# Optimization experiments

Hardware: AMD Instinct MI355X
Metric: run time of the kernel (lower is better)

Reference implementation:

```python
import jax, jax.numpy as jnp
import numpy as np

DIM = 512
HEADS = 8
HEAD_DIM = DIM // HEADS
SCALE = HEAD_DIM ** -0.5
LN_EPS = 1e-5


def _layernorm(t, g, b):
    mu = jnp.mean(t, axis=-1, keepdims=True)
    var = jnp.mean(jnp.square(t - mu), axis=-1, keepdims=True)
    return (t - mu) * jax.lax.rsqrt(var + LN_EPS) * g + b


def setup_inputs() -> dict:
    key = jax.random.key(0)
    ks = jax.random.split(key, 8)
    B, C, H, W = 2, DIM, 48, 48
    s = 1.0 / np.sqrt(DIM)
    return {
        "x": jax.random.normal(ks[0], (B, C, H, W), jnp.float32),
        "y": jax.random.normal(ks[1], (B, C, H, W), jnp.float32),
        # linear weights stored [in, out]
        "k_w": jax.random.uniform(ks[2], (DIM, DIM), jnp.float32, -s, s),
        "k_b": jax.random.uniform(ks[3], (DIM,), jnp.float32, -s, s),
        "qv_w": jax.random.uniform(ks[4], (DIM, 2 * DIM), jnp.float32, -s, s),
        "qv_b": jax.random.uniform(ks[5], (2 * DIM,), jnp.float32, -s, s),
        "lnx_g": jnp.ones((DIM,), jnp.float32),
        "lnx_b": jnp.zeros((DIM,), jnp.float32),
        "lny_g": jnp.ones((DIM,), jnp.float32),
        "lny_b": jnp.zeros((DIM,), jnp.float32),
    }


def _split_qv(t, qv_w, qv_b):
    B, N, C = t.shape
    qv = (t @ qv_w + qv_b).reshape(B, N, 2, HEADS, HEAD_DIM)
    qv = jnp.transpose(qv, (2, 0, 3, 1, 4))  # [2, B, h, N, d]
    return qv[0], qv[1]


def _heads(t):
    B, N, C = t.shape
    return jnp.transpose(t.reshape(B, N, HEADS, HEAD_DIM), (0, 2, 1, 3))  # [B,h,N,d]


def reference(x, y, k_w, k_b, qv_w, qv_b, lnx_g, lnx_b, lny_g, lny_b):
    B, C = x.shape[0], x.shape[1]
    xf = _layernorm(jnp.transpose(x.reshape(B, C, -1), (0, 2, 1)), lnx_g, lnx_b)  # [B,N,C]
    yf = _layernorm(jnp.transpose(y.reshape(B, C, -1), (0, 2, 1)), lny_g, lny_b)
    N = xf.shape[1]

    y_q, y_v = _split_qv(yf, qv_w, qv_b)
    x_q, x_v = _split_qv(xf, qv_w, qv_b)
    y_k = _heads(yf @ k_w + k_b)
    x_k = _heads(xf @ k_w + k_b)

    # branch 1: softmax(x_q y_k^T) x_v  -> standard [B,N,C]
    a1 = jax.nn.softmax(jnp.einsum('bhnd,bhmd->bhnm', x_q, y_k) * SCALE, axis=-1)
    xo = jnp.einsum('bhnm,bhmd->bhnd', a1, x_v)
    xo = jnp.transpose(xo, (0, 2, 1, 3)).reshape(B, N, C)

    # branch 2: faithful reproduction of torch quirk (x_k kept a leading 1-dim,
    # so the output [1,B,h,N,d].transpose(1,2).reshape(B,N,C) scrambles layout)
    a2 = jax.nn.softmax(jnp.einsum('bhnd,bhmd->bhnm', y_q, x_k) * SCALE, axis=-1)
    yo = jnp.einsum('bhnm,bhmd->bhnd', a2, y_v)  # [B,h,N,d]
    yo = jnp.transpose(yo[None], (0, 2, 1, 3, 4)).reshape(B, N, C)

    return jnp.concatenate([xo, yo], axis=0)  # [2B, N, C]
```

## Files before the change

### kernel.cpp

```cpp
#include <hip/hip_runtime.h>

#define DIM 512
#define NTOK 2304
#define HEADS 8
#define HD 64
#define LN_EPS 1e-5f
#define BNC 2359296
#define QSC 0.18033688011112042f

typedef __attribute__((ext_vector_type(8))) short short8;
typedef __attribute__((ext_vector_type(4))) short sh4;
typedef __attribute__((ext_vector_type(4))) float f32x4;

__device__ __forceinline__ short f2bf(float f) {
    union { float f; unsigned u; } x; x.f = f;
    unsigned r = (x.u + 0x7fffu + ((x.u >> 16) & 1u)) >> 16;
    return (short)(r & 0xffffu);
}
__device__ __forceinline__ unsigned fbits(float f) {
    union { float f; unsigned u; } x; x.f = f; return x.u;
}
__device__ __forceinline__ void gl2lds(const short* g, short* l) {
    __builtin_amdgcn_global_load_lds(
        (const __attribute__((address_space(1))) unsigned int*)g,
        (__attribute__((address_space(3))) unsigned int*)l, 16, 0, 0);
}

__global__ void k_pre(const float* __restrict__ x, const float* __restrict__ y,
                      const float* __restrict__ qv_w, const float* __restrict__ k_w,
                      const float* __restrict__ qv_b, const float* __restrict__ k_b,
                      const float* __restrict__ gx, const float* __restrict__ bx,
                      const float* __restrict__ gy, const float* __restrict__ by,
                      short* __restrict__ T, short* __restrict__ Wt,
                      float* __restrict__ bias) {
    __shared__ __align__(16) float tile[64][65];
    __shared__ float pS[4][64], pQ[4][64];
    __shared__ float muL[64], rsL[64];
    int bkid = blockIdx.x, tid = threadIdx.x;
    if (bkid < 1152) {
        int nt = bkid % 36, ct = (bkid / 36) % 8, sb = bkid / 288;
        int s = sb >> 1, b = sb & 1;
        int n0 = nt * 64, c0 = ct * 64;
        const float* src = (s ? y : x) + (size_t)b * DIM * NTOK;
        int nl = tid & 63, part = tid >> 6;
        {
            const float* p = src + n0 + nl;
            float sum = 0.f, sq = 0.f;
            for (int c = part * 128; c < part * 128 + 128; c++) {
                float v = p[(size_t)c * NTOK];
                sum += v; sq += v * v;
            }
            pS[part][nl] = sum; pQ[part][nl] = sq;
        }
        __syncthreads();
        if (tid < 64) {
            float ts = pS[0][tid] + pS[1][tid] + pS[2][tid] + pS[3][tid];
            float tq = pQ[0][tid] + pQ[1][tid] + pQ[2][tid] + pQ[3][tid];
            float m = ts * (1.0f / DIM);
            float var = tq * (1.0f / DIM) - m * m;
            muL[tid] = m;
            rsL[tid] = rsqrtf(var + LN_EPS);
        }
        for (int slot = tid; slot < 1024; slot += 256) {
            int r = slot >> 4, q = slot & 15;
            const float* p = src + (size_t)(c0 + r) * NTOK + n0 + q * 4;
            float4 v = *(const float4*)p;
            tile[r][q*4+0] = v.x; tile[r][q*4+1] = v.y;
            tile[r][q*4+2] = v.z; tile[r][q*4+3] = v.w;
        }
        __syncthreads();
        const float* g  = s ? gy : gx;
        const float* be = s ? by : bx;
        int nr = tid >> 2, cg = tid & 3;
        float m = muL[nr], r_ = rsL[nr];
        short8 o0, o1;
        for (int i = 0; i < 8; i++) {
            int c = c0 + cg * 16 + i;
            o0[i] = f2bf((tile[cg*16+i][nr] - m) * r_ * g[c] + be[c]);
        }
        for (int i = 0; i < 8; i++) {
            int c = c0 + cg * 16 + 8 + i;
            o1[i] = f2bf((tile[cg*16+8+i][nr] - m) * r_ * g[c] + be[c]);
        }
        short* dst = T + ((size_t)sb * NTOK + n0 + nr) * DIM + c0 + cg * 16;
        *(short8*)dst = o0;
        *(short8*)(dst + 8) = o1;
        return;
    }
    int idx = bkid - 1152;
    int jt = idx % 24, ct = idx / 24;
    int j0 = jt * 64, c0 = ct * 64;
    if (ct == 0 && tid < 64) {
        int j = j0 + tid;
        bias[j] = (j < 1024) ? qv_b[j] : k_b[j - 1024];
    }
    for (int slot = tid; slot < 1024; slot += 256) {
        int r = slot >> 4, q = slot & 15;
        int c = c0 + r;
        float4 v;
        if (j0 < 1024) v = *(const float4*)(qv_w + (size_t)c * 1024 + j0 + q * 4);
        else           v = *(const float4*)(k_w  + (size_t)c * 512  + (j0 - 1024) + q * 4);
        tile[r][q*4+0] = v.x; tile[r][q*4+1] = v.y;
        tile[r][q*4+2] = v.z; tile[r][q*4+3] = v.w;
    }
    __syncthreads();
    int jr = tid >> 2, cg = tid & 3;
    short8 o0, o1;
    for (int i = 0; i < 8; i++) o0[i] = f2bf(tile[cg*16+i][jr]);
    for (int i = 0; i < 8; i++) o1[i] = f2bf(tile[cg*16+8+i][jr]);
    short* dst = Wt + (size_t)(j0 + jr) * DIM + c0 + cg * 16;
    *(short8*)dst = o0;
    *(short8*)(dst + 8) = o1;
}

__global__ void __launch_bounds__(256)
k_gemm(const short* __restrict__ T, const short* __restrict__ Wt,
       const float* __restrict__ bias, short* __restrict__ QVK,
       short* __restrict__ VT) {
    __shared__ __align__(16) short smem[2 * 128 * 64];
    short* As = smem;
    short* Bs = smem + 128 * 64;
    int n0 = blockIdx.x * 128, j0 = blockIdx.y * 128, sb = blockIdx.z;
    int tid = threadIdx.x;
    int w = tid >> 6, l = tid & 63;
    int wr = w >> 1, wc = w & 1;
    int lrow = l & 15, quad = l >> 4;
    int r_in = (l >> 3) & 7, cc = l & 7;
    int ch = cc ^ r_in;
    int sw0 = (quad ^ (lrow & 7)) * 8;
    const short* Ab = T + (size_t)sb * NTOK * DIM;
    f32x4 acc[4][4] = {};
    for (int kk = 0; kk < 8; kk++) {
        if (kk) __syncthreads();
        for (int inst = 0; inst < 4; inst++) {
            int R = w * 32 + inst * 8 + r_in;
            gl2lds(Ab + (size_t)(n0 + R) * 512 + kk * 64 + ch * 8,
                   &As[(w * 32 + inst * 8) * 64]);
            gl2lds(Wt + (size_t)(j0 + R) * 512 + kk * 64 + ch * 8,
                   &Bs[(w * 32 + inst * 8) * 64]);
        }
        __syncthreads();
        for (int c2 = 0; c2 < 2; c2++) {
            int off = c2 ? (sw0 ^ 32) : sw0;
            short8 af[4], bf[4];
            for (int i = 0; i < 4; i++)
                af[i] = *(const short8*)&As[(wr*64 + i*16 + lrow) * 64 + off];
            for (int j = 0; j < 4; j++)
                bf[j] = *(const short8*)&Bs[(wc*64 + j*16 + lrow) * 64 + off];
            for (int i = 0; i < 4; i++)
                for (int j = 0; j < 4; j++)
                    acc[i][j] = __builtin_amdgcn_mfma_f32_16x16x32_bf16(af[i], bf[j], acc[i][j], 0, 0, 0);
        }
    }
    if (j0 >= 512 && j0 < 1024) {
        __syncthreads();
        for (int i = 0; i < 4; i++)
            for (int j = 0; j < 4; j++) {
                int jloc = wc * 64 + j * 16 + lrow;
                float bv = bias[j0 + jloc];
                int nloc = wr * 64 + i * 16 + quad * 4;
                int c8 = nloc >> 3, half = (nloc >> 2) & 1;
                sh4 pk;
                for (int reg = 0; reg < 4; reg++) pk[reg] = f2bf(acc[i][j][reg] + bv);
                *(sh4*)&smem[jloc * 128 + ((c8 ^ (jloc & 15)) * 8) + half * 4] = pk;
            }
        __syncthreads();
        for (int slot = tid; slot < 2048; slot += 256) {
            int row = slot >> 4, seg = slot & 15;
            short8 v = *(const short8*)&smem[row * 128 + ((seg ^ (row & 15)) * 8)];
            *(short8*)(VT + ((size_t)sb * 512 + (j0 - 512) + row) * NTOK + n0 + seg * 8) = v;
        }
    } else {
        for (int i = 0; i < 4; i++)
            for (int j = 0; j < 4; j++) {
                int jj = j0 + wc * 64 + j * 16 + lrow;
                float bv = bias[jj];
                float sc = (jj < 512) ? QSC : 1.0f;
                for (int reg = 0; reg < 4; reg++) {
                    int n = n0 + wr * 64 + i * 16 + quad * 4 + reg;
                    QVK[((size_t)sb * NTOK + n) * 1536 + jj] = f2bf((acc[i][j][reg] + bv) * sc);
                }
            }
    }
}

__global__ void __launch_bounds__(256)
k_attn(const short* __restrict__ QVK, const short* __restrict__ VT,
       float* __restrict__ out, float* __restrict__ O1,
       float* __restrict__ l0, float* __restrict__ l1) {
    __shared__ __align__(16) short Kbuf[2][64 * 64];
    __shared__ __align__(16) short Vbuf[2][64 * 64];
    __shared__ __align__(16) short Qs[64 * 64];
    int id = blockIdx.x;
    int half = id / 1152;
    int rid = id % 1152;
    int xcd = rid & 7, rem = rid >> 3;
    int qt = rem % 36, yhi = rem / 36;
    int yb = yhi * 8 + xcd;
    int br = yb >> 4;
    int b  = (yb >> 3) & 1;
    int h  = yb & 7;
    int tid = threadIdx.x;
    int w = tid >> 6, l = tid & 63;
    int lrow = l & 15, quad = l >> 4;
    int r_in = (l >> 3) & 7, cc = l & 7;
    int ch = cc ^ r_in;
    int sw0 = (quad ^ (lrow & 7)) * 8;
    int n0 = qt * 64;
    int m_base = half * 1152;
    const short* Qg = QVK + ((size_t)(br * 2 + b) * NTOK) * 1536 + h * 64;
    const short* Kg = QVK + ((size_t)((1 - br) * 2 + b) * NTOK) * 1536 + 1024 + h * 64;
    const short* Vg = VT + ((size_t)(br * 2 + b) * 512 + h * 64) * NTOK;

    for (int inst = 0; inst < 2; inst++) {
        int R = w * 16 + inst * 8 + r_in;
        gl2lds(Qg + (size_t)(n0 + R) * 1536 + ch * 8, &Qs[(w * 16 + inst * 8) * 64]);
    }

    const short* KnA = Kg + (size_t)(m_base + w * 16 + r_in) * 1536 + ch * 8;
    const short* KnB = Kg + (size_t)(m_base + w * 16 + 8 + r_in) * 1536 + ch * 8;
    const short* VnA = Vg + (size_t)(w * 16 + r_in) * NTOK + m_base + ch * 8;
    const short* VnB = Vg + (size_t)(w * 16 + 8 + r_in) * NTOK + m_base + ch * 8;
    int lds_off = l * 8;

    short8 ka = *(const short8*)(KnA);
    short8 kb = *(const short8*)(KnB);
    short8 va = *(const short8*)(VnA);
    short8 vb = *(const short8*)(VnB);
    KnA += (size_t)64 * 1536; KnB += (size_t)64 * 1536;
    VnA += 64; VnB += 64;

    __syncthreads();
    short8 bq0 = *(const short8*)&Qs[(w * 16 + lrow) * 64 + sw0];
    short8 bq1 = *(const short8*)&Qs[(w * 16 + lrow) * 64 + (sw0 ^ 32)];
    short* Pw = &Qs[w * 16 * 64];

    *(short8*)&Kbuf[0][(w * 16)     * 64 + lds_off] = ka;
    *(short8*)&Kbuf[0][(w * 16 + 8) * 64 + lds_off] = kb;
    *(short8*)&Vbuf[0][(w * 16)     * 64 + lds_off] = va;
    *(short8*)&Vbuf[0][(w * 16 + 8) * 64 + lds_off] = vb;
    ka = *(const short8*)(KnA);
    kb = *(const short8*)(KnB);
    va = *(const short8*)(VnA);
    vb = *(const short8*)(VnB);
    KnA += (size_t)64 * 1536; KnB += (size_t)64 * 1536;
    VnA += 64; VnB += 64;

    short8 ones;
    for (int i = 0; i < 8; i++) ones[i] = (short)0x3F80;

    f32x4 Oacc[4] = {};
    f32x4 lacc = {};
    int cur = 0;

    for (int mt = 0; mt < 18; mt++) {
        __syncthreads();
        const short* Ks = Kbuf[cur];
        const short* Vs = Vbuf[cur];

        for (int sub = 0; sub < 4; sub++) {
            short8 ak0 = *(const short8*)&Ks[(sub * 16 + lrow) * 64 + sw0];
            short8 ak1 = *(const short8*)&Ks[(sub * 16 + lrow) * 64 + (sw0 ^ 32)];
            f32x4 a = {};
            a = __builtin_amdgcn_mfma_f32_16x16x32_bf16(ak0, bq0, a, 0, 0, 0);
            a = __builtin_amdgcn_mfma_f32_16x16x32_bf16(ak1, bq1, a, 0, 0, 0);
            float p0 = __builtin_amdgcn_exp2f(a[0]), p1 = __builtin_amdgcn_exp2f(a[1]);
            float p2 = __builtin_amdgcn_exp2f(a[2]), p3 = __builtin_amdgcn_exp2f(a[3]);
            uint2 pk;
            pk.x = __builtin_amdgcn_perm(fbits(p1), fbits(p0), 0x07060302u);
            pk.y = __builtin_amdgcn_perm(fbits(p3), fbits(p2), 0x07060302u);
            *(uint2*)&Pw[lrow * 64 + (((2 * sub + (quad >> 1)) ^ (lrow & 7)) * 8) + (quad & 1) * 4] = pk;
        }

        short8 ap0 = *(const short8*)&Pw[lrow * 64 + sw0];
        short8 ap1 = *(const short8*)&Pw[lrow * 64 + (sw0 ^ 32)];
        lacc = __builtin_amdgcn_mfma_f32_16x16x32_bf16(ones, ap0, lacc, 0, 0, 0);
        lacc = __builtin_amdgcn_mfma_f32_16x16x32_bf16(ones, ap1, lacc, 0, 0, 0);
        for (int ddt = 0; ddt < 4; ddt++) {
            short8 av0 = *(const short8*)&Vs[(ddt * 16 + lrow) * 64 + sw0];
            short8 av1 = *(const short8*)&Vs[(ddt * 16 + lrow) * 64 + (sw0 ^ 32)];
            Oacc[ddt] = __builtin_amdgcn_mfma_f32_16x16x32_bf16(av0, ap0, Oacc[ddt], 0, 0, 0);
            Oacc[ddt] = __builtin_amdgcn_mfma_f32_16x16x32_bf16(av1, ap1, Oacc[ddt], 0, 0, 0);
        }

        if (mt + 1 < 18) {
            *(short8*)&Kbuf[cur ^ 1][(w * 16)     * 64 + lds_off] = ka;
            *(short8*)&Kbuf[cur ^ 1][(w * 16 + 8) * 64 + lds_off] = kb;
            *(short8*)&Vbuf[cur ^ 1][(w * 16)     * 64 + lds_off] = va;
            *(short8*)&Vbuf[cur ^ 1][(w * 16 + 8) * 64 + lds_off] = vb;
        }
        if (mt + 2 < 18) {
            ka = *(const short8*)(KnA);
            kb = *(const short8*)(KnB);
            va = *(const short8*)(VnA);
            vb = *(const short8*)(VnB);
        }
        KnA += (size_t)64 * 1536; KnB += (size_t)64 * 1536;
        VnA += 64; VnB += 64;
        cur ^= 1;
    }

    int n = n0 + w * 16 + lrow;
    if (quad == 0) (half ? l1 : l0)[yb * NTOK + n] = lacc[0];
    for (int ddt = 0; ddt < 4; ddt++) {
        float4 o;
        o.x = Oacc[ddt][0];
        o.y = Oacc[ddt][1];
        o.z = Oacc[ddt][2];
        o.w = Oacc[ddt][3];
        if (half == 0) {
            if (br == 0)
                *(float4*)&out[((size_t)b * NTOK + n) * 512 + h * 64 + ddt * 16 + quad * 4] = o;
            else
                *(float4*)&out[(size_t)BNC + ((size_t)(h * 2 + b) * NTOK + n) * 64 + ddt * 16 + quad * 4] = o;
        } else {
            *(float4*)&O1[((size_t)yb * NTOK + n) * 64 + ddt * 16 + quad * 4] = o;
        }
    }
}

__global__ void __launch_bounds__(256)
k_norm(float* __restrict__ out, const float* __restrict__ O1,
       const float* __restrict__ l0, const float* __restrict__ l1) {
    int i = blockIdx.x * 256 + threadIdx.x;
    int o = i * 4;
    int yb, n, d;
    if (o < BNC) {
        int b = o / (NTOK * 512);
        int r = o % (NTOK * 512);
        n = r >> 9;
        int c = r & 511;
        d = c & 63;
        yb = b * 8 + (c >> 6);
    } else {
        int o2 = o - BNC;
        int hb = o2 / (NTOK * 64);
        n = (o2 >> 6) % NTOK;
        d = o2 & 63;
        yb = 16 + (hb & 1) * 8 + (hb >> 1);
    }
    int li = yb * NTOK + n;
    float linv = 1.f / (l0[li] + l1[li]);
    float4 a = *(const float4*)&out[o];
    float4 q = *(const float4*)&O1[(size_t)li * 64 + d];
    a.x = (a.x + q.x) * linv;
    a.y = (a.y + q.y) * linv;
    a.z = (a.z + q.z) * linv;
    a.w = (a.w + q.w) * linv;
    *(float4*)&out[o] = a;
}

extern "C" void kernel_launch(void* const* d_in, const int* in_sizes, int n_in,
                              void* d_out, int out_size, void* d_ws, size_t ws_size,
                              hipStream_t stream) {
    const float* x     = (const float*)d_in[0];
    const float* y     = (const float*)d_in[1];
    const float* k_w   = (const float*)d_in[2];
    const float* k_b   = (const float*)d_in[3];
    const float* qv_w  = (const float*)d_in[4];
    const float* qv_b  = (const float*)d_in[5];
    const float* lnx_g = (const float*)d_in[6];
    const float* lnx_b = (const float*)d_in[7];
    const float* lny_g = (const float*)d_in[8];
    const float* lny_b = (const float*)d_in[9];
    float* out = (float*)d_out;

    char* ws = (char*)d_ws;
    float* bias = (float*)ws;
    short* T    = (short*)(ws + 6144);
    short* Wt   = T + 4718592;
    short* QVK  = Wt + 786432;
    short* VT   = QVK + 14155776;
    float* O1   = (float*)(ws + 48764928);
    float* l0   = (float*)(ws + 67639296);
    float* l1   = (float*)(ws + 67934208);

    k_pre  <<<1344, 256, 0, stream>>>(x, y, qv_w, k_w, qv_b, k_b,
                                      lnx_g, lnx_b, lny_g, lny_b, T, Wt, bias);
    k_gemm <<<dim3(18, 12, 4), 256, 0, stream>>>(T, Wt, bias, QVK, VT);
    k_attn <<<2304, 256, 0, stream>>>(QVK, VT, out, O1, l0, l1);
    k_norm <<<4608, 256, 0, stream>>>(out, O1, l0, l1);
}
```

Before: 200.3 us.

## Double-buffer GEMM LDS tiles and swap MFMA operands for vectorized epilogue stores

The projection GEMM now keeps two LDS buffers for the A and B tiles. It issues the global-to-LDS loads for the next k-slice before computing on the current one, so load latency overlaps MFMA work, and each iteration needs one barrier instead of two. The MFMA operands are swapped, which transposes the accumulator layout so each lane holds four consecutive output columns. The QVK epilogue can then write packed 4-element bf16 stores and load the bias as a float4. This doubles the GEMM's LDS footprint, which may lower occupancy.

```diff
diff --git a/kernel.cpp b/kernel.cpp
--- a/kernel.cpp
+++ b/kernel.cpp
@@ -117,9 +117,8 @@
 k_gemm(const short* __restrict__ T, const short* __restrict__ Wt,
        const float* __restrict__ bias, short* __restrict__ QVK,
        short* __restrict__ VT) {
-    __shared__ __align__(16) short smem[2 * 128 * 64];
-    short* As = smem;
-    short* Bs = smem + 128 * 64;
+    __shared__ __align__(16) short Abuf[2][128 * 64];
+    __shared__ __align__(16) short Bbuf[2][128 * 64];
     int n0 = blockIdx.x * 128, j0 = blockIdx.y * 128, sb = blockIdx.z;
     int tid = threadIdx.x;
     int w = tid >> 6, l = tid & 63;
@@ -130,57 +129,85 @@
     int sw0 = (quad ^ (lrow & 7)) * 8;
     const short* Ab = T + (size_t)sb * NTOK * DIM;
     f32x4 acc[4][4] = {};
+
+    #pragma unroll
+    for (int inst = 0; inst < 4; inst++) {
+        int R = w * 32 + inst * 8 + r_in;
+        gl2lds(Ab + (size_t)(n0 + R) * 512 + 0 * 64 + ch * 8, &Abuf[0][(w * 32 + inst * 8) * 64]);
+        gl2lds(Wt + (size_t)(j0 + R) * 512 + 0 * 64 + ch * 8, &Bbuf[0][(w * 32 + inst * 8) * 64]);
+    }
+    int cur = 0;
     for (int kk = 0; kk < 8; kk++) {
-        if (kk) __syncthreads();
-        for (int inst = 0; inst < 4; inst++) {
-            int R = w * 32 + inst * 8 + r_in;
-            gl2lds(Ab + (size_t)(n0 + R) * 512 + kk * 64 + ch * 8,
-                   &As[(w * 32 + inst * 8) * 64]);
-            gl2lds(Wt + (size_t)(j0 + R) * 512 + kk * 64 + ch * 8,
-                   &Bs[(w * 32 + inst * 8) * 64]);
-        }
-        __syncthreads();
+        __syncthreads();
+        if (kk + 1 < 8) {
+            #pragma unroll
+            for (int inst = 0; inst < 4; inst++) {
+                int R = w * 32 + inst * 8 + r_in;
+                gl2lds(Ab + (size_t)(n0 + R) * 512 + (kk + 1) * 64 + ch * 8,
+                       &Abuf[cur ^ 1][(w * 32 + inst * 8) * 64]);
+                gl2lds(Wt + (size_t)(j0 + R) * 512 + (kk + 1) * 64 + ch * 8,
+                       &Bbuf[cur ^ 1][(w * 32 + inst * 8) * 64]);
+            }
+        }
+        #pragma unroll
         for (int c2 = 0; c2 < 2; c2++) {
             int off = c2 ? (sw0 ^ 32) : sw0;
             short8 af[4], bf[4];
+            #pragma unroll
             for (int i = 0; i < 4; i++)
-                af[i] = *(const short8*)&As[(wr*64 + i*16 + lrow) * 64 + off];
+                af[i] = *(const short8*)&Abuf[cur][(wr*64 + i*16 + lrow) * 64 + off];
+            #pragma unroll
             for (int j = 0; j < 4; j++)
-                bf[j] = *(const short8*)&Bs[(wc*64 + j*16 + lrow) * 64 + off];
+                bf[j] = *(const short8*)&Bbuf[cur][(wc*64 + j*16 + lrow) * 64 + off];
+            #pragma unroll
             for (int i = 0; i < 4; i++)
+                #pragma unroll
                 for (int j = 0; j < 4; j++)
-                    acc[i][j] = __builtin_amdgcn_mfma_f32_16x16x32_bf16(af[i], bf[j], acc[i][j], 0, 0, 0);
-        }
+                    acc[i][j] = __builtin_amdgcn_mfma_f32_16x16x32_bf16(bf[j], af[i], acc[i][j], 0, 0, 0);
+        }
+        cur ^= 1;
     }
     if (j0 >= 512 && j0 < 1024) {
         __syncthreads();
+        short* sm = &Abuf[0][0];
+        #pragma unroll
         for (int i = 0; i < 4; i++)
+            #pragma unroll
             for (int j = 0; j < 4; j++) {
-                int jloc = wc * 64 + j * 16 + lrow;
-                float bv = bias[j0 + jloc];
-                int nloc = wr * 64 + i * 16 + quad * 4;
-                int c8 = nloc >> 3, half = (nloc >> 2) & 1;
-                sh4 pk;
-                for (int reg = 0; reg < 4; reg++) pk[reg] = f2bf(acc[i][j][reg] + bv);
-                *(sh4*)&smem[jloc * 128 + ((c8 ^ (jloc & 15)) * 8) + half * 4] = pk;
+                int jb = wc * 64 + j * 16 + quad * 4;
+                int nloc = wr * 64 + i * 16 + lrow;
+                float4 bv4 = *(const float4*)&bias[j0 + jb];
+                float bvs[4] = {bv4.x, bv4.y, bv4.z, bv4.w};
+                #pragma unroll
+                for (int reg = 0; reg < 4; reg++) {
+                    int jloc = jb + reg;
+                    sm[jloc * 128 + (((nloc >> 3) ^ (jloc & 15)) * 8) + (nloc & 7)]
+                        = f2bf(acc[i][j][reg] + bvs[reg]);
+                }
             }
         __syncthreads();
         for (int slot = tid; slot < 2048; slot += 256) {
             int row = slot >> 4, seg = slot & 15;
-            short8 v = *(const short8*)&smem[row * 128 + ((seg ^ (row & 15)) * 8)];
+            short8 v = *(const short8*)&sm[row * 128 + ((seg ^ (row & 15)) * 8)];
             *(short8*)(VT + ((size_t)sb * 512 + (j0 - 512) + row) * NTOK + n0 + seg * 8) = v;
         }
     } else {
-        for (int i = 0; i < 4; i++)
+        #pragma unroll
+        for (int i = 0; i < 4; i++) {
+            int n = n0 + wr * 64 + i * 16 + lrow;
+            #pragma unroll
             for (int j = 0; j < 4; j++) {
-                int jj = j0 + wc * 64 + j * 16 + lrow;
-                float bv = bias[jj];
-                float sc = (jj < 512) ? QSC : 1.0f;
-                for (int reg = 0; reg < 4; reg++) {
-                    int n = n0 + wr * 64 + i * 16 + quad * 4 + reg;
-                    QVK[((size_t)sb * NTOK + n) * 1536 + jj] = f2bf((acc[i][j][reg] + bv) * sc);
-                }
+                int jjb = j0 + wc * 64 + j * 16 + quad * 4;
+                float4 bv4 = *(const float4*)&bias[jjb];
+                float bvs[4] = {bv4.x, bv4.y, bv4.z, bv4.w};
+                float sc = (jjb < 512) ? QSC : 1.0f;
+                sh4 pk;
+                #pragma unroll
+                for (int reg = 0; reg < 4; reg++)
+                    pk[reg] = f2bf((acc[i][j][reg] + bvs[reg]) * sc);
+                *(sh4*)&QVK[((size_t)sb * NTOK + n) * 1536 + jjb] = pk;
             }
+        }
     }
 }
 
```

After: 203.9 us. No clear change (+1.8%).
